# Performance work log

Measured on AMD Instinct MI355X. Metric: run time of the kernel, lower is better.

## Reference

```python
import jax, jax.numpy as jnp
import numpy as np
from jax import lax

B, F, I, S = 4, 1024, 2048, 2048
K, G = 7, 4
INIT_SCALE = 1.0
LEAK = 0.02


def _norm(x):
    # normalize over channel dim (axis 1): subtract mean, divide by RMS-style L2 norm
    x = x - jnp.mean(x, axis=1, keepdims=True)
    n = jnp.sqrt(jnp.sum(x * x, axis=1, keepdims=True)) * (x.shape[1] ** -0.5)
    return x / (n + 1e-5)


def _conv1x1(x, w):
    # x: [B, Cin, S], w: [Cout, Cin, 1]
    return jnp.einsum('bcs,oc->bos', x, w[:, :, 0])


def setup_inputs() -> dict:
    key = jax.random.key(0)
    k1, k2, k3, k4 = jax.random.split(key, 4)
    inp = jax.random.normal(k1, (B, F, S), dtype=jnp.float32)
    divisor = (jnp.arange(S, dtype=jnp.float32) + 1.0).reshape(1, 1, S)
    w0_gate = jax.random.normal(k2, (3 * I, F, 1), dtype=jnp.float32) * (F ** -0.5)
    w1 = jax.random.normal(k3, (3 * I, I // G, K), dtype=jnp.float32) * ((I // G * K) ** -0.5)
    w2_gate = jax.random.normal(k4, (F, I, 1), dtype=jnp.float32) * (I ** -0.5)
    return {"inp": inp, "divisor": divisor, "w0_gate": w0_gate, "w1": w1, "w2_gate": w2_gate}


def reference(inp, divisor, w0_gate, w1, w2_gate):
    # 1x1 conv features -> 3*intermediate
    x = _conv1x1(inp, w0_gate)                       # [B, 3I, S]
    depth, scale, shift = jnp.split(x, 3, axis=1)    # each [B, I, S]
    cum = jnp.cumsum(depth, axis=-1)
    x = jax.nn.leaky_relu(_norm(cum / divisor * scale + shift), LEAK)
    # causal pad + grouped conv1d intermediate -> 3*intermediate
    x = jnp.pad(x, ((0, 0), (0, 0), (K - 1, 0)))
    x = lax.conv_general_dilated(x, w1, window_strides=(1,), padding='VALID',
                                 dimension_numbers=('NCH', 'OIH', 'NCH'),
                                 feature_group_count=G)  # [B, 3I, S]
    s0, s1, sh = jnp.split(x, 3, axis=1)
    x = jax.nn.leaky_relu(_norm(s0 * s1 + sh), LEAK)     # [B, I, S]
    # 1x1 conv intermediate -> features
    out = _conv1x1(x, w2_gate)                           # [B, F, S]
    return out * INIT_SCALE
```

## Files before the change

kernel.cpp:

```cpp
#include <hip/hip_runtime.h>

#define BATCH 4
#define FDIM  1024
#define IDIM  2048
#define SDIM  2048
#define I3    6144
#define KW    7
#define IG    512
#define OG    1536
#define KD2   3584
#define SP    2056

using short8 = __attribute__((ext_vector_type(8))) short;
using f32x4  = __attribute__((ext_vector_type(4))) float;

__device__ __forceinline__ unsigned short f2bf(float f) {
  unsigned int u = __float_as_uint(f);
  u += 0x7fffu + ((u >> 16) & 1u);
  return (unsigned short)(u >> 16);
}
__device__ __forceinline__ float bf2f(unsigned short u) {
  return __uint_as_float((unsigned int)u << 16);
}

__device__ __forceinline__ void gload16(const void* g, void* l) {
  __builtin_amdgcn_global_load_lds((const __attribute__((address_space(1))) void*)g,
                                   (__attribute__((address_space(3))) void*)l,
                                   16, 0, 0);
}

template<int MODE, int OBF16>
__global__ __launch_bounds__(512, 1)
void gemm256(const unsigned short* __restrict__ A,
             const unsigned short* __restrict__ Bt,
             void* __restrict__ C,
             int mtiles, int ktiles,
             int lda, int ldb, int ldc,
             long aZ, long bZ, long cZ)
{
  __shared__ unsigned short lds[2][2][16384];

  const int tid  = threadIdx.x;
  const int wv   = tid >> 6;
  const int lane = tid & 63;
  const int lr = lane & 15, lq = lane >> 4;
  const int wr = wv >> 2, wc = wv & 3;
  const int xm = (lr & 7) << 4;
  const int c8 = ((tid & 7) ^ ((tid >> 3) & 7)) << 3;

  const int nwg = gridDim.x;
  const int cpx = nwg >> 3;
  const int bid = blockIdx.x;
  const int w   = (bid & 7) * cpx + (bid >> 3);
  const int T   = mtiles << 3;
  const int z   = w / T;
  const int rr  = w - z * T;
  const int mt  = rr % mtiles;
  const int nt  = rr / mtiles;

  const unsigned short* Ab;
  const unsigned short* Bb;
  size_t coff;
  int gbase = 0;
  if (MODE == 2) {
    int b = z >> 2, g = z & 3;
    Ab = A + (size_t)g * OG * KD2;
    Bb = Bt + (size_t)b * SP * IDIM;
    coff = ((size_t)b * I3 + (size_t)g * OG) * (size_t)ldc;
    gbase = g * IG;
  } else {
    Ab = A + (size_t)z * aZ;
    Bb = Bt + (size_t)z * bZ;
    coff = (size_t)z * cZ;
  }

  const int m0 = mt * 256, n0 = nt * 256;

  f32x4 acc[8][4];
  const f32x4 vzero = {0.f, 0.f, 0.f, 0.f};
#pragma unroll
  for (int i = 0; i < 8; ++i)
#pragma unroll
    for (int j = 0; j < 4; ++j) acc[i][j] = vzero;

  auto STAGEC = [&](int buf, int kt1, int c) {
    const int k0 = kt1 << 6;
    int row = (c << 6) + (tid >> 3);
    gload16(Ab + (size_t)(m0 + row) * lda + (k0 + c8),
            &lds[buf][0][c * 4096 + wv * 512]);
    const unsigned short* g;
    if (MODE == 2) {
      int kk = k0 + c8;
      g = Bb + (size_t)(n0 + row + (kk >> 9) + 2) * IDIM + (gbase + (kk & 511));
    } else {
      g = Bb + (size_t)(n0 + row) * ldb + (k0 + c8);
    }
    gload16(g, &lds[buf][1][c * 4096 + wv * 512]);
  };

  auto RDA = [&](int buf, int i, int kk) -> short8 {
    int row = wr * 128 + i * 16 + lr;
    int off = ((row << 7) + (kk << 1) + (lq << 4)) ^ xm;
    return *(const short8*)((const char*)&lds[buf][0][0] + off);
  };
  auto RDB = [&](int buf, int j, int kk) -> short8 {
    int row = wc * 64 + j * 16 + lr;
    int off = ((row << 7) + (kk << 1) + (lq << 4)) ^ xm;
    return *(const short8*)((const char*)&lds[buf][1][0] + off);
  };

#define MFMA16(AF, BV, IOFF)                                                     \
  __builtin_amdgcn_s_setprio(1);                                                 \
  _Pragma("unroll")                                                              \
  for (int i = 0; i < 4; ++i)                                                    \
    _Pragma("unroll")                                                            \
    for (int j = 0; j < 4; ++j)                                                  \
      acc[i + IOFF][j] =                                                         \
          __builtin_amdgcn_mfma_f32_16x16x32_bf16(AF[i], BV[j], acc[i + IOFF][j],\
                                                  0, 0, 0);                      \
  __builtin_amdgcn_s_setprio(0);

  STAGEC(0, 0, 0); STAGEC(0, 0, 1); STAGEC(0, 0, 2); STAGEC(0, 0, 3);
  asm volatile("s_waitcnt vmcnt(0)" ::: "memory");
  __builtin_amdgcn_s_barrier();
  __builtin_amdgcn_sched_barrier(0);

  for (int kt = 0; kt < ktiles - 1; ++kt) {
    const int cur = kt & 1;
    short8 af0[4], af1[4], bv0[4], bv1[4];
#pragma unroll
    for (int j = 0; j < 4; ++j) bv0[j] = RDB(cur, j, 0);
#pragma unroll
    for (int i = 0; i < 4; ++i) af0[i] = RDA(cur, i, 0);
    STAGEC(cur ^ 1, kt + 1, 0);
#pragma unroll
    for (int i = 0; i < 4; ++i) af1[i] = RDA(cur, i + 4, 0);
    MFMA16(af0, bv0, 0)
    STAGEC(cur ^ 1, kt + 1, 1);
#pragma unroll
    for (int j = 0; j < 4; ++j) bv1[j] = RDB(cur, j, 32);
#pragma unroll
    for (int i = 0; i < 4; ++i) af0[i] = RDA(cur, i, 32);
    MFMA16(af1, bv0, 4)
    STAGEC(cur ^ 1, kt + 1, 2);
#pragma unroll
    for (int i = 0; i < 4; ++i) af1[i] = RDA(cur, i + 4, 32);
    MFMA16(af0, bv1, 0)
    STAGEC(cur ^ 1, kt + 1, 3);
    MFMA16(af1, bv1, 4)

    asm volatile("s_waitcnt vmcnt(0)" ::: "memory");
    __builtin_amdgcn_s_barrier();
    __builtin_amdgcn_sched_barrier(0);
  }

  {
    const int cur = (ktiles - 1) & 1;
    short8 af0[4], af1[4], bv0[4], bv1[4];
#pragma unroll
    for (int j = 0; j < 4; ++j) bv0[j] = RDB(cur, j, 0);
#pragma unroll
    for (int i = 0; i < 4; ++i) af0[i] = RDA(cur, i, 0);
#pragma unroll
    for (int i = 0; i < 4; ++i) af1[i] = RDA(cur, i + 4, 0);
    MFMA16(af0, bv0, 0)
#pragma unroll
    for (int j = 0; j < 4; ++j) bv1[j] = RDB(cur, j, 32);
#pragma unroll
    for (int i = 0; i < 4; ++i) af0[i] = RDA(cur, i, 32);
    MFMA16(af1, bv0, 4)
#pragma unroll
    for (int i = 0; i < 4; ++i) af1[i] = RDA(cur, i + 4, 32);
    MFMA16(af0, bv1, 0)
    MFMA16(af1, bv1, 4)
  }
#undef MFMA16

#pragma unroll
  for (int i = 0; i < 8; ++i) {
#pragma unroll
    for (int j = 0; j < 4; ++j) {
      int ccol  = n0 + wc * 64 + j * 16 + lr;
      int rbase = m0 + wr * 128 + i * 16 + lq * 4;
      if (OBF16) {
        unsigned short* Cs = (unsigned short*)C + coff;
#pragma unroll
        for (int e = 0; e < 4; ++e)
          Cs[(size_t)(rbase + e) * ldc + ccol] = f2bf(acc[i][j][e]);
      } else {
        float* Cf = (float*)C + coff;
#pragma unroll
        for (int e = 0; e < 4; ++e)
          Cf[(size_t)(rbase + e) * ldc + ccol] = acc[i][j][e];
      }
    }
  }
}

__global__ __launch_bounds__(256, 2)
void gemm128(const unsigned short* __restrict__ A,
             const unsigned short* __restrict__ Bt,
             float* __restrict__ C,
             int mtiles, int ktiles,
             int lda, int ldb, int ldc,
             long aZ, long bZ, long cZ)
{
  __shared__ unsigned short sA[128 * 64];
  __shared__ unsigned short sB[128 * 64];

  const int tid  = threadIdx.x;
  const int wave = tid >> 6;
  const int lane = tid & 63;
  const int mt = blockIdx.x % mtiles;
  const int nt = blockIdx.x / mtiles;
  const int z  = blockIdx.y;

  const unsigned short* Ab = A + (size_t)z * aZ;
  const unsigned short* Bb = Bt + (size_t)z * bZ;
  float* Cb = C + (size_t)z * cZ;

  const int m0 = mt * 128, n0 = nt * 128;
  const int wr = wave >> 1, wc = wave & 1;
  const int lr = lane & 15, lq = lane >> 4;
  const int xm = (lr & 7) << 4;
  const int c8 = ((tid & 7) ^ ((tid >> 3) & 7)) << 3;

  f32x4 acc[4][4];
  const f32x4 vzero = {0.f, 0.f, 0.f, 0.f};
#pragma unroll
  for (int i = 0; i < 4; ++i)
#pragma unroll
    for (int j = 0; j < 4; ++j) acc[i][j] = vzero;

  for (int kt = 0; kt < ktiles; ++kt) {
    const int k0 = kt * 64;
#pragma unroll
    for (int it = 0; it < 4; ++it) {
      int row = it * 32 + (tid >> 3);
      gload16(Ab + (size_t)(m0 + row) * lda + (k0 + c8),
              &sA[(size_t)(it * 256 + (tid & ~63)) * 8]);
    }
#pragma unroll
    for (int it = 0; it < 4; ++it) {
      int row = it * 32 + (tid >> 3);
      gload16(Bb + (size_t)(n0 + row) * ldb + (k0 + c8),
              &sB[(size_t)(it * 256 + (tid & ~63)) * 8]);
    }
    asm volatile("s_waitcnt vmcnt(0)" ::: "memory");
    __builtin_amdgcn_s_barrier();
#pragma unroll
    for (int kk = 0; kk < 64; kk += 32) {
      short8 af[4], bfr[4];
#pragma unroll
      for (int i = 0; i < 4; ++i) {
        int row = wr * 64 + i * 16 + lr;
        af[i] = *(const short8*)((const char*)sA + (((row << 7) + (kk << 1) + (lq << 4)) ^ xm));
      }
#pragma unroll
      for (int j = 0; j < 4; ++j) {
        int row = wc * 64 + j * 16 + lr;
        bfr[j] = *(const short8*)((const char*)sB + (((row << 7) + (kk << 1) + (lq << 4)) ^ xm));
      }
#pragma unroll
      for (int i = 0; i < 4; ++i)
#pragma unroll
        for (int j = 0; j < 4; ++j)
          acc[i][j] = __builtin_amdgcn_mfma_f32_16x16x32_bf16(af[i], bfr[j], acc[i][j], 0, 0, 0);
    }
    __builtin_amdgcn_s_barrier();
  }

#pragma unroll
  for (int i = 0; i < 4; ++i) {
#pragma unroll
    for (int j = 0; j < 4; ++j) {
      int ccol  = n0 + wc * 64 + j * 16 + lr;
      int rbase = m0 + wr * 64 + i * 16 + lq * 4;
#pragma unroll
      for (int e = 0; e < 4; ++e)
        Cb[(size_t)(rbase + e) * ldc + ccol] = acc[i][j][e];
    }
  }
}

__global__ void cvt_f2b(const float* __restrict__ in, unsigned short* __restrict__ out, long n) {
  long stride = (long)gridDim.x * blockDim.x;
  for (long i = (long)blockIdx.x * blockDim.x + threadIdx.x; i < n; i += stride)
    out[i] = f2bf(in[i]);
}

__global__ void perm_w1(const float* __restrict__ in, unsigned short* __restrict__ out) {
  __shared__ float row[2][KD2];
  int o0 = blockIdx.x * 2;
  int t  = threadIdx.x;
#pragma unroll
  for (int r = 0; r < 2; ++r)
    for (int j = t; j < KD2; j += 256)
      row[r][j] = in[(size_t)(o0 + r) * KD2 + j];
  __syncthreads();
#pragma unroll
  for (int r = 0; r < 2; ++r)
    for (int j = t; j < KD2; j += 256) {
      int c = j & 511, k = j >> 9;
      out[(size_t)(o0 + r) * KD2 + j] = f2bf(row[r][c * KW + k]);
    }
}

__global__ void transpose_in(const float* __restrict__ in, unsigned short* __restrict__ out) {
  __shared__ float tile[64][65];
  int bid = blockIdx.x;
  int b   = bid >> 9;
  int rem = bid & 511;
  int ft  = rem >> 5;
  int st  = rem & 31;
  int tc  = threadIdx.x & 63, tr = threadIdx.x >> 6;
  const float* ip = in + ((size_t)b * FDIM + ft * 64) * SDIM + st * 64;
#pragma unroll
  for (int r = tr; r < 64; r += 4)
    tile[r][tc] = ip[(size_t)r * SDIM + tc];
  __syncthreads();
  unsigned short* op = out + ((size_t)b * SDIM + st * 64) * FDIM + ft * 64;
#pragma unroll
  for (int r = tr; r < 64; r += 4)
    op[(size_t)r * FDIM + tc] = f2bf(tile[tc][r]);
}

__global__ void scan_rows(const unsigned short* __restrict__ C1, unsigned short* __restrict__ V) {
  int rid = blockIdx.x;
  int b = rid >> 11;
  int i = rid & 2047;
  const unsigned short* dp = C1 + ((size_t)b * I3 + i) * SDIM;
  const unsigned short* sp = dp + (size_t)IDIM * SDIM;
  const unsigned short* hp = dp + (size_t)2 * IDIM * SDIM;
  unsigned short* vp = V + ((size_t)b * IDIM + i) * SDIM;
  int t = threadIdx.x, lane = t & 63, wid = t >> 6;

  short8 dv = *(const short8*)(dp + t * 8);
  float c[8];
  float run = 0.f;
#pragma unroll
  for (int e = 0; e < 8; ++e) { run += bf2f((unsigned short)dv[e]); c[e] = run; }

  float s = run;
#pragma unroll
  for (int off = 1; off < 64; off <<= 1) {
    float v = __shfl_up(s, off, 64);
    if (lane >= off) s += v;
  }
  __shared__ float wtot[4];
  if (lane == 63) wtot[wid] = s;
  __syncthreads();
  float base = 0.f;
#pragma unroll
  for (int w2 = 0; w2 < 3; ++w2) base += (w2 < wid) ? wtot[w2] : 0.f;
  float excl = base + s - run;

  short8 sv = *(const short8*)(sp + t * 8);
  short8 hv = *(const short8*)(hp + t * 8);
  short8 ov;
#pragma unroll
  for (int e = 0; e < 8; ++e) {
    int si = t * 8 + e;
    float val = (excl + c[e]) / (float)(si + 1) * bf2f((unsigned short)sv[e]) + bf2f((unsigned short)hv[e]);
    ov[e] = (short)f2bf(val);
  }
  *(short8*)(vp + t * 8) = ov;
}

template<int MODE>
__global__ void stats_part(const unsigned short* __restrict__ X, float* __restrict__ psum,
                           float* __restrict__ psq) {
  int bid = blockIdx.x;
  int b   = bid >> 5;
  int s0  = (bid & 31) * 64;
  int iz  = blockIdx.y;
  int ts  = threadIdx.x & 63, tg = threadIdx.x >> 6;
  float sum = 0.f, sq = 0.f;
  for (int i = iz * 512 + tg; i < iz * 512 + 512; i += 4) {
    float g;
    if (MODE == 1) {
      g = bf2f(X[((size_t)b * IDIM + i) * SDIM + s0 + ts]);
    } else {
      float a  = bf2f(X[((size_t)b * I3 + i) * SDIM + s0 + ts]);
      float bb = bf2f(X[((size_t)b * I3 + IDIM + i) * SDIM + s0 + ts]);
      float cc = bf2f(X[((size_t)b * I3 + 2 * IDIM + i) * SDIM + s0 + ts]);
      g = a * bb + cc;
    }
    sum += g; sq += g * g;
  }
  __shared__ float sS[4][64], sQ[4][64];
  sS[tg][ts] = sum; sQ[tg][ts] = sq;
  __syncthreads();
  if (threadIdx.x < 64) {
    float s = sS[0][ts] + sS[1][ts] + sS[2][ts] + sS[3][ts];
    float q = sQ[0][ts] + sQ[1][ts] + sQ[2][ts] + sQ[3][ts];
    psum[((size_t)b * SDIM + s0 + ts) * 4 + iz] = s;
    psq [((size_t)b * SDIM + s0 + ts) * 4 + iz] = q;
  }
}

__global__ void stats_final(const float* __restrict__ psum, const float* __restrict__ psq,
                            float* __restrict__ mean, float* __restrict__ inv) {
  int idx = blockIdx.x * 256 + threadIdx.x;
  if (idx >= BATCH * SDIM) return;
  float s = psum[idx * 4] + psum[idx * 4 + 1] + psum[idx * 4 + 2] + psum[idx * 4 + 3];
  float q = psq [idx * 4] + psq [idx * 4 + 1] + psq [idx * 4 + 2] + psq [idx * 4 + 3];
  float m   = s * (1.f / 2048.f);
  float var = q * (1.f / 2048.f) - m * m;
  float n   = sqrtf(fmaxf(var, 0.f));
  mean[idx] = m;
  inv[idx]  = 1.f / (n + 1e-5f);
}

template<int MODE>
__global__ void norm_apply(const unsigned short* __restrict__ X, const float* __restrict__ mean,
                           const float* __restrict__ inv, unsigned short* __restrict__ out) {
  __shared__ float tile[64][65];
  int bid = blockIdx.x;
  int b   = bid >> 5;
  int s0  = (bid & 31) * 64;
  int i0  = blockIdx.y * 512;
  int tc  = threadIdx.x & 63, tr = threadIdx.x >> 6;
  float mn = mean[(size_t)b * SDIM + s0 + tc];
  float iv = inv [(size_t)b * SDIM + s0 + tc];
  size_t orow = (MODE == 1) ? ((size_t)b * SP + 8 + s0) : ((size_t)b * SDIM + s0);
  for (int ic = i0; ic < i0 + 512; ic += 64) {
#pragma unroll
    for (int r = tr; r < 64; r += 4) {
      int i = ic + r;
      float g;
      if (MODE == 1) {
        g = bf2f(X[((size_t)b * IDIM + i) * SDIM + s0 + tc]);
      } else {
        float a  = bf2f(X[((size_t)b * I3 + i) * SDIM + s0 + tc]);
        float bb = bf2f(X[((size_t)b * I3 + IDIM + i) * SDIM + s0 + tc]);
        float cc = bf2f(X[((size_t)b * I3 + 2 * IDIM + i) * SDIM + s0 + tc]);
        g = a * bb + cc;
      }
      float y = (g - mn) * iv;
      y = (y >= 0.f) ? y : 0.02f * y;
      tile[r][tc] = y;
    }
    __syncthreads();
#pragma unroll
    for (int r = tr; r < 64; r += 4)
      out[(orow + r) * IDIM + ic + tc] = f2bf(tile[tc][r]);
    __syncthreads();
  }
}

__global__ void zero_x1t_pad(unsigned short* __restrict__ x1t) {
  int idx = blockIdx.x * 256 + threadIdx.x;
  if (idx < BATCH * 8 * IDIM) {
    int b   = idx / (8 * IDIM);
    int rem = idx - b * (8 * IDIM);
    x1t[(size_t)b * SP * IDIM + rem] = 0;
  }
}

__global__ void report_ws(float* __restrict__ out, float mb) {
  if (threadIdx.x == 0 && blockIdx.x == 0) out[0] = mb;
}

extern "C" void kernel_launch(void* const* d_in, const int* in_sizes, int n_in,
                              void* d_out, int out_size, void* d_ws, size_t ws_size,
                              hipStream_t stream) {
  const float* inp = (const float*)d_in[0];
  const float* w0  = (const float*)d_in[2];
  const float* w1  = (const float*)d_in[3];
  const float* w2  = (const float*)d_in[4];
  float* out = (float*)d_out;
  char* ws = (char*)d_ws;

  const size_t REQ = 216465408ULL;
  if (ws_size < REQ) {
    report_ws<<<1, 1, 0, stream>>>(out, (float)(ws_size >> 20));
    return;
  }

  unsigned short* A2   = (unsigned short*)(ws + 0);
  unsigned short* A3   = (unsigned short*)(ws + 44040192);
  unsigned short* C1   = (unsigned short*)(ws + 48234496);
  unsigned short* X1T  = (unsigned short*)(ws + 148897792);
  char*           VXr  = ws + 182583296;
  unsigned short* A1   = (unsigned short*)(VXr + 0);
  unsigned short* BINT = (unsigned short*)(VXr + 12582912);
  unsigned short* V    = (unsigned short*)(VXr + 0);
  unsigned short* X2T  = (unsigned short*)(VXr + 0);
  float* PSUM = (float*)(ws + 216137728);
  float* PSQ  = (float*)(ws + 216268800);
  float* MEAN = (float*)(ws + 216399872);
  float* INV  = (float*)(ws + 216432640);

  cvt_f2b<<<2048, 256, 0, stream>>>(w0, A1, (long)I3 * FDIM);
  cvt_f2b<<<2048, 256, 0, stream>>>(w2, A3, (long)FDIM * IDIM);
  perm_w1<<<I3 / 2, 256, 0, stream>>>(w1, A2);
  transpose_in<<<2048, 256, 0, stream>>>(inp, BINT);
  zero_x1t_pad<<<256, 256, 0, stream>>>(X1T);

  gemm256<0, 1><<<24 * 8 * BATCH, 512, 0, stream>>>(
      A1, BINT, C1, 24, 16, FDIM, FDIM, SDIM,
      0L, (long)SDIM * FDIM, (long)I3 * SDIM);

  scan_rows<<<BATCH * IDIM, 256, 0, stream>>>(C1, V);

  stats_part<1><<<dim3(128, 4), 256, 0, stream>>>(V, PSUM, PSQ);
  stats_final<<<32, 256, 0, stream>>>(PSUM, PSQ, MEAN, INV);
  norm_apply<1><<<dim3(128, 4), 256, 0, stream>>>(V, MEAN, INV, X1T);

  gemm256<2, 1><<<6 * 8 * 16, 512, 0, stream>>>(
      A2, X1T, C1, 6, 56, KD2, 0, SDIM, 0L, 0L, 0L);

  stats_part<2><<<dim3(128, 4), 256, 0, stream>>>(C1, PSUM, PSQ);
  stats_final<<<32, 256, 0, stream>>>(PSUM, PSQ, MEAN, INV);
  norm_apply<2><<<dim3(128, 4), 256, 0, stream>>>(C1, MEAN, INV, X2T);

  gemm128<<<dim3(8 * 16, BATCH), 256, 0, stream>>>(
      A3, X2T, out, 8, 32, IDIM, IDIM, SDIM,
      0L, (long)SDIM * IDIM, (long)FDIM * SDIM);
}
```

Measured before the change: 674.8 us.

## Switch gemm256 to 32x32 MFMA, fuse stats_final into norm_apply, cache gated product

The 256x256 GEMM now uses 32x32x16 bf16 MFMA tiles with 4x2 f32x16 accumulators instead of 16x16x32 tiles. This cuts LDS fragment reads per MFMA, and the launch bound is raised to allow two blocks per CU. The stats_final launches are removed and norm_apply reduces the partial sums itself. stats_part<2> also writes the gated product s0*s1+sh as bf16, so norm_apply reads one tensor instead of three. The costs are an extra 33MB write, possible register pressure from the occupancy hint, and reuse of the X1T region as scratch.

```diff
diff --git a/kernel.cpp b/kernel.cpp
--- a/kernel.cpp
+++ b/kernel.cpp
@@ -13,6 +13,7 @@
 
 using short8 = __attribute__((ext_vector_type(8))) short;
 using f32x4  = __attribute__((ext_vector_type(4))) float;
+using f32x16 = __attribute__((ext_vector_type(16))) float;
 
 __device__ __forceinline__ unsigned short f2bf(float f) {
   unsigned int u = __float_as_uint(f);
@@ -30,7 +31,7 @@
 }
 
 template<int MODE, int OBF16>
-__global__ __launch_bounds__(512, 1)
+__global__ __launch_bounds__(512, 2)
 void gemm256(const unsigned short* __restrict__ A,
              const unsigned short* __restrict__ Bt,
              void* __restrict__ C,
@@ -43,9 +44,9 @@
   const int tid  = threadIdx.x;
   const int wv   = tid >> 6;
   const int lane = tid & 63;
-  const int lr = lane & 15, lq = lane >> 4;
+  const int l31  = lane & 31;
+  const int kh16 = (lane >> 5) << 4;
   const int wr = wv >> 2, wc = wv & 3;
-  const int xm = (lr & 7) << 4;
   const int c8 = ((tid & 7) ^ ((tid >> 3) & 7)) << 3;
 
   const int nwg = gridDim.x;
@@ -76,12 +77,13 @@
 
   const int m0 = mt * 256, n0 = nt * 256;
 
-  f32x4 acc[8][4];
-  const f32x4 vzero = {0.f, 0.f, 0.f, 0.f};
-#pragma unroll
-  for (int i = 0; i < 8; ++i)
-#pragma unroll
-    for (int j = 0; j < 4; ++j) acc[i][j] = vzero;
+  f32x16 acc[4][2];
+#pragma unroll
+  for (int i = 0; i < 4; ++i)
+#pragma unroll
+    for (int j = 0; j < 2; ++j)
+#pragma unroll
+      for (int e = 0; e < 16; ++e) acc[i][j][e] = 0.f;
 
   auto STAGEC = [&](int buf, int kt1, int c) {
     const int k0 = kt1 << 6;
@@ -98,25 +100,31 @@
     gload16(g, &lds[buf][1][c * 4096 + wv * 512]);
   };
 
-  auto RDA = [&](int buf, int i, int kk) -> short8 {
-    int row = wr * 128 + i * 16 + lr;
-    int off = ((row << 7) + (kk << 1) + (lq << 4)) ^ xm;
+  auto RDA32 = [&](int buf, int i, int s) -> short8 {
+    int row = wr * 128 + i * 32 + l31;
+    int off = (row << 7) + (((s << 5) + kh16) ^ ((row & 7) << 4));
     return *(const short8*)((const char*)&lds[buf][0][0] + off);
   };
-  auto RDB = [&](int buf, int j, int kk) -> short8 {
-    int row = wc * 64 + j * 16 + lr;
-    int off = ((row << 7) + (kk << 1) + (lq << 4)) ^ xm;
+  auto RDB32 = [&](int buf, int j, int s) -> short8 {
+    int row = wc * 64 + j * 32 + l31;
+    int off = (row << 7) + (((s << 5) + kh16) ^ ((row & 7) << 4));
     return *(const short8*)((const char*)&lds[buf][1][0] + off);
   };
 
-#define MFMA16(AF, BV, IOFF)                                                     \
+#define RDSET(AF, BV, BUF, S)                                  \
+  _Pragma("unroll")                                            \
+  for (int i = 0; i < 4; ++i) AF[i] = RDA32(BUF, i, S);        \
+  _Pragma("unroll")                                            \
+  for (int j = 0; j < 2; ++j) BV[j] = RDB32(BUF, j, S);
+
+#define MFMA8(AF, BV)                                                            \
   __builtin_amdgcn_s_setprio(1);                                                 \
   _Pragma("unroll")                                                              \
   for (int i = 0; i < 4; ++i)                                                    \
     _Pragma("unroll")                                                            \
-    for (int j = 0; j < 4; ++j)                                                  \
-      acc[i + IOFF][j] =                                                         \
-          __builtin_amdgcn_mfma_f32_16x16x32_bf16(AF[i], BV[j], acc[i + IOFF][j],\
+    for (int j = 0; j < 2; ++j)                                                  \
+      acc[i][j] =                                                                \
+          __builtin_amdgcn_mfma_f32_32x32x16_bf16(AF[i], BV[j], acc[i][j],       \
                                                   0, 0, 0);                      \
   __builtin_amdgcn_s_setprio(0);
 
@@ -127,27 +135,19 @@
 
   for (int kt = 0; kt < ktiles - 1; ++kt) {
     const int cur = kt & 1;
-    short8 af0[4], af1[4], bv0[4], bv1[4];
-#pragma unroll
-    for (int j = 0; j < 4; ++j) bv0[j] = RDB(cur, j, 0);
-#pragma unroll
-    for (int i = 0; i < 4; ++i) af0[i] = RDA(cur, i, 0);
+    short8 af0[4], af1[4], bv0[2], bv1[2];
+    RDSET(af0, bv0, cur, 0)
     STAGEC(cur ^ 1, kt + 1, 0);
-#pragma unroll
-    for (int i = 0; i < 4; ++i) af1[i] = RDA(cur, i + 4, 0);
-    MFMA16(af0, bv0, 0)
+    RDSET(af1, bv1, cur, 1)
+    MFMA8(af0, bv0)
     STAGEC(cur ^ 1, kt + 1, 1);
-#pragma unroll
-    for (int j = 0; j < 4; ++j) bv1[j] = RDB(cur, j, 32);
-#pragma unroll
-    for (int i = 0; i < 4; ++i) af0[i] = RDA(cur, i, 32);
-    MFMA16(af1, bv0, 4)
+    RDSET(af0, bv0, cur, 2)
+    MFMA8(af1, bv1)
     STAGEC(cur ^ 1, kt + 1, 2);
-#pragma unroll
-    for (int i = 0; i < 4; ++i) af1[i] = RDA(cur, i + 4, 32);
-    MFMA16(af0, bv1, 0)
+    RDSET(af1, bv1, cur, 3)
+    MFMA8(af0, bv0)
     STAGEC(cur ^ 1, kt + 1, 3);
-    MFMA16(af1, bv1, 4)
+    MFMA8(af1, bv1)
 
     asm volatile("s_waitcnt vmcnt(0)" ::: "memory");
     __builtin_amdgcn_s_barrier();
@@ -156,42 +156,35 @@
 
   {
     const int cur = (ktiles - 1) & 1;
-    short8 af0[4], af1[4], bv0[4], bv1[4];
-#pragma unroll
-    for (int j = 0; j < 4; ++j) bv0[j] = RDB(cur, j, 0);
-#pragma unroll
-    for (int i = 0; i < 4; ++i) af0[i] = RDA(cur, i, 0);
-#pragma unroll
-    for (int i = 0; i < 4; ++i) af1[i] = RDA(cur, i + 4, 0);
-    MFMA16(af0, bv0, 0)
-#pragma unroll
-    for (int j = 0; j < 4; ++j) bv1[j] = RDB(cur, j, 32);
-#pragma unroll
-    for (int i = 0; i < 4; ++i) af0[i] = RDA(cur, i, 32);
-    MFMA16(af1, bv0, 4)
-#pragma unroll
-    for (int i = 0; i < 4; ++i) af1[i] = RDA(cur, i + 4, 32);
-    MFMA16(af0, bv1, 0)
-    MFMA16(af1, bv1, 4)
-  }
-#undef MFMA16
-
-#pragma unroll
-  for (int i = 0; i < 8; ++i) {
-#pragma unroll
-    for (int j = 0; j < 4; ++j) {
-      int ccol  = n0 + wc * 64 + j * 16 + lr;
-      int rbase = m0 + wr * 128 + i * 16 + lq * 4;
+    short8 af0[4], af1[4], bv0[2], bv1[2];
+    RDSET(af0, bv0, cur, 0)
+    RDSET(af1, bv1, cur, 1)
+    MFMA8(af0, bv0)
+    RDSET(af0, bv0, cur, 2)
+    MFMA8(af1, bv1)
+    RDSET(af1, bv1, cur, 3)
+    MFMA8(af0, bv0)
+    MFMA8(af1, bv1)
+  }
+#undef MFMA8
+#undef RDSET
+
+#pragma unroll
+  for (int i = 0; i < 4; ++i) {
+#pragma unroll
+    for (int j = 0; j < 2; ++j) {
+      int ccol  = n0 + wc * 64 + j * 32 + l31;
+      int rbase = m0 + wr * 128 + i * 32 + ((lane >> 5) << 2);
       if (OBF16) {
         unsigned short* Cs = (unsigned short*)C + coff;
 #pragma unroll
-        for (int e = 0; e < 4; ++e)
-          Cs[(size_t)(rbase + e) * ldc + ccol] = f2bf(acc[i][j][e]);
+        for (int r = 0; r < 16; ++r)
+          Cs[(size_t)(rbase + (r & 3) + ((r >> 2) << 3)) * ldc + ccol] = f2bf(acc[i][j][r]);
       } else {
         float* Cf = (float*)C + coff;
 #pragma unroll
-        for (int e = 0; e < 4; ++e)
-          Cf[(size_t)(rbase + e) * ldc + ccol] = acc[i][j][e];
+        for (int r = 0; r < 16; ++r)
+          Cf[(size_t)(rbase + (r & 3) + ((r >> 2) << 3)) * ldc + ccol] = acc[i][j][r];
       }
     }
   }
@@ -369,7 +362,7 @@
 
 template<int MODE>
 __global__ void stats_part(const unsigned short* __restrict__ X, float* __restrict__ psum,
-                           float* __restrict__ psq) {
+                           float* __restrict__ psq, unsigned short* __restrict__ G) {
   int bid = blockIdx.x;
   int b   = bid >> 5;
   int s0  = (bid & 31) * 64;
@@ -385,6 +378,7 @@
       float bb = bf2f(X[((size_t)b * I3 + IDIM + i) * SDIM + s0 + ts]);
       float cc = bf2f(X[((size_t)b * I3 + 2 * IDIM + i) * SDIM + s0 + ts]);
       g = a * bb + cc;
+      G[((size_t)b * IDIM + i) * SDIM + s0 + ts] = f2bf(g);
     }
     sum += g; sq += g * g;
   }
@@ -399,44 +393,27 @@
   }
 }
 
-__global__ void stats_final(const float* __restrict__ psum, const float* __restrict__ psq,
-                            float* __restrict__ mean, float* __restrict__ inv) {
-  int idx = blockIdx.x * 256 + threadIdx.x;
-  if (idx >= BATCH * SDIM) return;
-  float s = psum[idx * 4] + psum[idx * 4 + 1] + psum[idx * 4 + 2] + psum[idx * 4 + 3];
-  float q = psq [idx * 4] + psq [idx * 4 + 1] + psq [idx * 4 + 2] + psq [idx * 4 + 3];
-  float m   = s * (1.f / 2048.f);
-  float var = q * (1.f / 2048.f) - m * m;
-  float n   = sqrtf(fmaxf(var, 0.f));
-  mean[idx] = m;
-  inv[idx]  = 1.f / (n + 1e-5f);
-}
-
 template<int MODE>
-__global__ void norm_apply(const unsigned short* __restrict__ X, const float* __restrict__ mean,
-                           const float* __restrict__ inv, unsigned short* __restrict__ out) {
+__global__ void norm_apply(const unsigned short* __restrict__ X, const float* __restrict__ psum,
+                           const float* __restrict__ psq, unsigned short* __restrict__ out) {
   __shared__ float tile[64][65];
   int bid = blockIdx.x;
   int b   = bid >> 5;
   int s0  = (bid & 31) * 64;
   int i0  = blockIdx.y * 512;
   int tc  = threadIdx.x & 63, tr = threadIdx.x >> 6;
-  float mn = mean[(size_t)b * SDIM + s0 + tc];
-  float iv = inv [(size_t)b * SDIM + s0 + tc];
+  size_t sidx = ((size_t)b * SDIM + s0 + tc) * 4;
+  float s4 = psum[sidx] + psum[sidx + 1] + psum[sidx + 2] + psum[sidx + 3];
+  float q4 = psq [sidx] + psq [sidx + 1] + psq [sidx + 2] + psq [sidx + 3];
+  float mn  = s4 * (1.f / 2048.f);
+  float var = q4 * (1.f / 2048.f) - mn * mn;
+  float iv  = 1.f / (sqrtf(fmaxf(var, 0.f)) + 1e-5f);
   size_t orow = (MODE == 1) ? ((size_t)b * SP + 8 + s0) : ((size_t)b * SDIM + s0);
   for (int ic = i0; ic < i0 + 512; ic += 64) {
 #pragma unroll
     for (int r = tr; r < 64; r += 4) {
       int i = ic + r;
-      float g;
-      if (MODE == 1) {
-        g = bf2f(X[((size_t)b * IDIM + i) * SDIM + s0 + tc]);
-      } else {
-        float a  = bf2f(X[((size_t)b * I3 + i) * SDIM + s0 + tc]);
-        float bb = bf2f(X[((size_t)b * I3 + IDIM + i) * SDIM + s0 + tc]);
-        float cc = bf2f(X[((size_t)b * I3 + 2 * IDIM + i) * SDIM + s0 + tc]);
-        g = a * bb + cc;
-      }
+      float g = bf2f(X[((size_t)b * IDIM + i) * SDIM + s0 + tc]);
       float y = (g - mn) * iv;
       y = (y >= 0.f) ? y : 0.02f * y;
       tile[r][tc] = y;
@@ -482,6 +459,7 @@
   unsigned short* A3   = (unsigned short*)(ws + 44040192);
   unsigned short* C1   = (unsigned short*)(ws + 48234496);
   unsigned short* X1T  = (unsigned short*)(ws + 148897792);
+  unsigned short* G    = (unsigned short*)(ws + 148897792);
   char*           VXr  = ws + 182583296;
   unsigned short* A1   = (unsigned short*)(VXr + 0);
   unsigned short* BINT = (unsigned short*)(VXr + 12582912);
@@ -489,8 +467,6 @@
   unsigned short* X2T  = (unsigned short*)(VXr + 0);
   float* PSUM = (float*)(ws + 216137728);
   float* PSQ  = (float*)(ws + 216268800);
-  float* MEAN = (float*)(ws + 216399872);
-  float* INV  = (float*)(ws + 216432640);
 
   cvt_f2b<<<2048, 256, 0, stream>>>(w0, A1, (long)I3 * FDIM);
   cvt_f2b<<<2048, 256, 0, stream>>>(w2, A3, (long)FDIM * IDIM);
@@ -504,16 +480,14 @@
 
   scan_rows<<<BATCH * IDIM, 256, 0, stream>>>(C1, V);
 
-  stats_part<1><<<dim3(128, 4), 256, 0, stream>>>(V, PSUM, PSQ);
-  stats_final<<<32, 256, 0, stream>>>(PSUM, PSQ, MEAN, INV);
-  norm_apply<1><<<dim3(128, 4), 256, 0, stream>>>(V, MEAN, INV, X1T);
+  stats_part<1><<<dim3(128, 4), 256, 0, stream>>>(V, PSUM, PSQ, nullptr);
+  norm_apply<1><<<dim3(128, 4), 256, 0, stream>>>(V, PSUM, PSQ, X1T);
 
   gemm256<2, 1><<<6 * 8 * 16, 512, 0, stream>>>(
       A2, X1T, C1, 6, 56, KD2, 0, SDIM, 0L, 0L, 0L);
 
-  stats_part<2><<<dim3(128, 4), 256, 0, stream>>>(C1, PSUM, PSQ);
-  stats_final<<<32, 256, 0, stream>>>(PSUM, PSQ, MEAN, INV);
-  norm_apply<2><<<dim3(128, 4), 256, 0, stream>>>(C1, MEAN, INV, X2T);
+  stats_part<2><<<dim3(128, 4), 256, 0, stream>>>(C1, PSUM, PSQ, G);
+  norm_apply<2><<<dim3(128, 4), 256, 0, stream>>>(G, PSUM, PSQ, X2T);
 
   gemm128<<<dim3(8 * 16, BATCH), 256, 0, stream>>>(
       A3, X2T, out, 8, 32, IDIM, IDIM, SDIM,
```

Result: slower. 721.1 us (+6.9%).
